# Optimization experiments

Measured on AMD Instinct MI355X. Metric: run time of the kernel, lower is better.

## Reference

```python
import math
import jax, jax.numpy as jnp
import numpy as np

B, T, D = 8, 2048, 1024

def _gelu(x):
    # tanh-approx GELU, matching the torch module's _gelu
    c = math.sqrt(2.0 / math.pi)
    return 0.5 * x * (1.0 + jnp.tanh(c * (x + 0.044715 * x * x * x)))

def _normalize(x, axis):
    # matches F.normalize(eps=1e-12)
    n = jnp.linalg.norm(x, axis=axis, keepdims=True)
    return x / jnp.maximum(n, 1e-12)

def setup_inputs() -> dict:
    key = jax.random.key(0)
    k1, k2 = jax.random.split(key)
    x = jax.random.normal(k1, (B, T, D), dtype=jnp.float32)
    ema_out = _normalize(jax.random.normal(k2, (D,), dtype=jnp.float32), 0)[..., 0] if False else None
    ema = jax.random.normal(k2, (D,), dtype=jnp.float32)
    ema = ema / jnp.maximum(jnp.linalg.norm(ema), 1e-12)
    return {
        "x": x,
        "ema_out": ema,
        "logit_decay": jnp.float32(math.log(0.9 / 0.1)),
        "log_tau": jnp.float32(math.log(2.0)),
        "log_blend": jnp.float32(math.log(0.3 / 0.7)),
        "logit_blend_seq": jnp.float32(0.0),
    }

def reference(x, ema_out, logit_decay, log_tau, log_blend, logit_blend_seq):
    Bx, Tx, Dx = x.shape
    tau = jnp.exp(log_tau)
    alpha = jax.nn.sigmoid(log_blend)
    w_seq = jax.nn.sigmoid(logit_blend_seq)

    out = _gelu(x)                              # [B,T,D]
    out_norm = _normalize(out, -1)              # [B,T,D]
    ema_norm = ema_out / jnp.maximum(jnp.linalg.norm(ema_out), 1e-12)  # [D]

    ema_sim = jnp.einsum('btd,d->bt', out_norm, ema_norm)             # [B,T]
    sim_mat = jnp.einsum('btd,bsd->bts', out_norm, out_norm)          # [B,T,T]

    causal = jnp.tril(jnp.ones((Tx, Tx), dtype=bool), k=-1)           # strict past
    sim_past = jnp.where(causal[None], sim_mat, -2.0)
    seq_sim = jnp.max(sim_past, axis=-1)                              # [B,T]

    has_past = (jnp.arange(Tx) > 0)[None, :]                          # [1,T]
    seq_sim = jnp.where(has_past, seq_sim, ema_sim)

    familiarity = w_seq * seq_sim + (1.0 - w_seq) * ema_sim
    novelty = jnp.exp(-tau * familiarity)
    gate = 1.0 - alpha + alpha * novelty                              # [B,T]
    return out * gate[..., None]
```

## Files before the change

kernel.cpp:

```cpp
#include <hip/hip_runtime.h>
#include <math.h>

#define NB 8
#define TT 2048
#define DD 1024
#define NTI 16
#define NPAIR 136

typedef __attribute__((ext_vector_type(4))) float floatx4;

__device__ inline float fast_gelu(float x) {
    float z = 0.7978845608028654f * (x + 0.044715f * x * x * x);
    float e = __expf(2.0f * z);
    float th = 1.0f - 2.0f / (e + 1.0f);
    return 0.5f * x * (1.0f + th);
}

__global__ __launch_bounds__(256) void k_gelu_norm(
        const float* __restrict__ x, const float* __restrict__ ema,
        unsigned int* __restrict__ onrm8, float* __restrict__ ema_sim) {
    int row = blockIdx.x * 4 + (threadIdx.x >> 6);
    int lane = threadIdx.x & 63;
    const float4* xr = reinterpret_cast<const float4*>(x + (size_t)row * DD);
    const float4* er = reinterpret_cast<const float4*>(ema);
    float g[16];
    float ss = 0.f, dt = 0.f, e2 = 0.f;
#pragma unroll
    for (int j = 0; j < 4; ++j) {
        float4 v = xr[j * 64 + lane];
        float4 e = er[j * 64 + lane];
        float vv[4] = {v.x, v.y, v.z, v.w};
        float ee[4] = {e.x, e.y, e.z, e.w};
        e2 += ee[0] * ee[0] + ee[1] * ee[1] + ee[2] * ee[2] + ee[3] * ee[3];
#pragma unroll
        for (int i = 0; i < 4; ++i) {
            float o = fast_gelu(vv[i]);
            g[j * 4 + i] = o;
            ss += o * o;
            dt += o * ee[i];
        }
    }
#pragma unroll
    for (int m = 1; m < 64; m <<= 1) {
        ss += __shfl_xor(ss, m);
        dt += __shfl_xor(dt, m);
        e2 += __shfl_xor(e2, m);
    }
    float inv = 1.0f / fmaxf(sqrtf(ss), 1e-12f);
    float einv = 1.0f / fmaxf(sqrtf(e2), 1e-12f);
    unsigned int* o8 = onrm8 + (size_t)row * (DD / 4);
#pragma unroll
    for (int j = 0; j < 4; ++j) {
        int pk = 0;
        pk = __builtin_amdgcn_cvt_pk_fp8_f32(g[j * 4 + 0] * inv, g[j * 4 + 1] * inv, pk, false);
        pk = __builtin_amdgcn_cvt_pk_fp8_f32(g[j * 4 + 2] * inv, g[j * 4 + 3] * inv, pk, true);
        o8[j * 64 + lane] = (unsigned int)pk;
    }
    if (lane == 0) ema_sim[row] = dt * inv * einv;
}

__global__ __launch_bounds__(256) void k_seqmax(const unsigned char* __restrict__ onrm8,
                                                float* __restrict__ part) {
    __shared__ __align__(16) unsigned char lds[32768];

    int id = blockIdx.x;
    int nid = (id & 7) * NPAIR + (id >> 3);
    int b = nid / NPAIR;
    int p = nid % NPAIR;
    int ti = (int)((sqrtf(8.0f * (float)p + 1.0f) - 1.0f) * 0.5f);
    while ((ti + 1) * (ti + 2) / 2 <= p) ++ti;
    while (ti * (ti + 1) / 2 > p) --ti;
    int sj = p - ti * (ti + 1) / 2;

    int lane = threadIdx.x & 63;
    int wave = threadIdx.x >> 6;
    int wr = wave >> 1, wc = wave & 1;
    int rl = lane & 15, g = lane >> 4;

    const unsigned char* Abase = onrm8 + (size_t)(b * TT + ti * 128) * DD;
    const unsigned char* Bbase = onrm8 + (size_t)(b * TT + sj * 128) * DD;

    floatx4 acc[4][4];
#pragma unroll
    for (int i = 0; i < 4; i++)
#pragma unroll
        for (int j = 0; j < 4; j++) acc[i][j] = (floatx4){0.f, 0.f, 0.f, 0.f};

    auto stage = [&](int kt) {
#pragma unroll
        for (int i = 0; i < 4; ++i) {
            int c = wave * 4 + i;
            int off = c * 1024 + lane * 16;
            int row = off >> 7;
            int colb = (off & 127) ^ ((row & 7) << 4);
            const unsigned char* srcA = Abase + (size_t)row * DD + kt * 128 + colb;
            const unsigned char* srcB = Bbase + (size_t)row * DD + kt * 128 + colb;
            __builtin_amdgcn_global_load_lds(
                (const __attribute__((address_space(1))) unsigned int*)srcA,
                (__attribute__((address_space(3))) unsigned int*)(&lds[0] + c * 1024),
                16, 0, 0);
            __builtin_amdgcn_global_load_lds(
                (const __attribute__((address_space(1))) unsigned int*)srcB,
                (__attribute__((address_space(3))) unsigned int*)(&lds[16384] + c * 1024),
                16, 0, 0);
        }
    };

    auto ldfrag = [&](const unsigned char* base, int r, int ks) -> long {
        int sw = (r & 7) << 4;
        return *(const long*)(base + r * 128 + ((ks * 32 + g * 8) ^ sw));
    };

    for (int kt = 0; kt < 8; ++kt) {
        stage(kt);
        __syncthreads();
#pragma unroll
        for (int ks = 0; ks < 4; ++ks) {
            long af[4], bg[4];
#pragma unroll
            for (int f = 0; f < 4; ++f) {
                af[f] = ldfrag(&lds[0], wr * 64 + f * 16 + rl, ks);
                bg[f] = ldfrag(&lds[16384], wc * 64 + f * 16 + rl, ks);
            }
#pragma unroll
            for (int fi = 0; fi < 4; ++fi)
#pragma unroll
                for (int fj = 0; fj < 4; ++fj)
                    acc[fi][fj] = __builtin_amdgcn_mfma_f32_16x16x32_fp8_fp8(
                        af[fi], bg[fj], acc[fi][fj], 0, 0, 0);
        }
        __syncthreads();
    }

    int t0g = ti * 128 + wr * 64;
    int s0g = sj * 128 + wc * 64;
#pragma unroll
    for (int fi = 0; fi < 4; ++fi) {
#pragma unroll
        for (int r = 0; r < 4; ++r) {
            int trow = t0g + fi * 16 + g * 4 + r;
            float m = -2.0f;
#pragma unroll
            for (int fj = 0; fj < 4; ++fj) {
                int scol = s0g + fj * 16 + rl;
                m = fmaxf(m, (scol < trow) ? acc[fi][fj][r] : -2.0f);
            }
#pragma unroll
            for (int msk = 1; msk < 16; msk <<= 1) m = fmaxf(m, __shfl_xor(m, msk));
            if (rl == 0)
                part[(((size_t)b * 32 + sj * 2 + wc) << 11) + trow] = m;
        }
    }
}

__global__ __launch_bounds__(256) void k_gate(
        const float* __restrict__ x, float* __restrict__ out,
        const float* __restrict__ ema_sim, const float* __restrict__ part,
        const float* __restrict__ log_tau,
        const float* __restrict__ log_blend,
        const float* __restrict__ logit_blend_seq) {
    int row = blockIdx.x * 4 + (threadIdx.x >> 6);
    int lane = threadIdx.x & 63;
    int b = row >> 11;
    int t = row & (TT - 1);

    int n = 2 * ((t >> 7) + 1);
    float m = (lane < n) ? part[(((size_t)b * 32 + lane) << 11) + t] : -2.0f;
#pragma unroll
    for (int msk = 1; msk < 64; msk <<= 1) m = fmaxf(m, __shfl_xor(m, msk));

    float tau = __expf(log_tau[0]);
    float alpha = 1.f / (1.f + __expf(-log_blend[0]));
    float wseq = 1.f / (1.f + __expf(-logit_blend_seq[0]));
    float es = ema_sim[row];
    float sq = (t > 0) ? m : es;
    float fam = wseq * sq + (1.f - wseq) * es;
    float gate = 1.f - alpha + alpha * __expf(-tau * fam);

    const float4* xr = reinterpret_cast<const float4*>(x + (size_t)row * DD);
    float4* orow = reinterpret_cast<float4*>(out + (size_t)row * DD);
#pragma unroll
    for (int j = 0; j < 4; ++j) {
        float4 v = xr[j * 64 + lane];
        float4 o;
        o.x = fast_gelu(v.x) * gate;
        o.y = fast_gelu(v.y) * gate;
        o.z = fast_gelu(v.z) * gate;
        o.w = fast_gelu(v.w) * gate;
        orow[j * 64 + lane] = o;
    }
}

extern "C" void kernel_launch(void* const* d_in, const int* in_sizes, int n_in,
                              void* d_out, int out_size, void* d_ws, size_t ws_size,
                              hipStream_t stream) {
    const float* x = (const float*)d_in[0];
    const float* ema = (const float*)d_in[1];
    const float* log_tau = (const float*)d_in[3];
    const float* log_blend = (const float*)d_in[4];
    const float* logit_bs = (const float*)d_in[5];
    float* out = (float*)d_out;

    char* ws = (char*)d_ws;
    float* ema_sim = (float*)(ws + (4 << 10));
    float* part = (float*)(ws + (132 << 10));
    unsigned char* onrm8 = (unsigned char*)(ws + ((size_t)2304 << 10));

    k_gelu_norm<<<NB * TT / 4, 256, 0, stream>>>(x, ema, (unsigned int*)onrm8, ema_sim);
    k_seqmax<<<NB * NPAIR, 256, 0, stream>>>(onrm8, part);
    k_gate<<<NB * TT / 4, 256, 0, stream>>>(x, out, ema_sim, part,
                                            log_tau, log_blend, logit_bs);
}
```

Before: 90.12 us.

## Use single-wave 64x64 tiles with double-buffered LDS prefetch in seqmax

The causal similarity-max kernel now launches one wave per block, each computing a 64x64 lower-triangular tile, instead of four waves sharing a 128x128 tile. Without cross-wave sharing the block barriers go away, and the next K slice is prefetched into a second LDS buffer with explicit vmcnt waits so loads overlap MFMA work. The smaller tiles waste less compute on the diagonal and give more blocks, but each block reuses its loaded data less, so global/L2 traffic rises. The gate kernel is updated to reduce over 64-row partials.

```diff
diff --git a/kernel.cpp b/kernel.cpp
--- a/kernel.cpp
+++ b/kernel.cpp
@@ -4,8 +4,8 @@
 #define NB 8
 #define TT 2048
 #define DD 1024
-#define NTI 16
-#define NPAIR 136
+#define NT64 32
+#define NP64 528
 
 typedef __attribute__((ext_vector_type(4))) float floatx4;
 
@@ -59,26 +59,24 @@
     if (lane == 0) ema_sim[row] = dt * inv * einv;
 }
 
-__global__ __launch_bounds__(256) void k_seqmax(const unsigned char* __restrict__ onrm8,
-                                                float* __restrict__ part) {
-    __shared__ __align__(16) unsigned char lds[32768];
+__global__ __launch_bounds__(64) void k_seqmax(const unsigned char* __restrict__ onrm8,
+                                               float* __restrict__ part) {
+    __shared__ __align__(16) unsigned char lds[2][16384];
 
     int id = blockIdx.x;
-    int nid = (id & 7) * NPAIR + (id >> 3);
-    int b = nid / NPAIR;
-    int p = nid % NPAIR;
+    int nid = (id & 7) * NP64 + (id >> 3);
+    int b = nid / NP64;
+    int p = nid % NP64;
     int ti = (int)((sqrtf(8.0f * (float)p + 1.0f) - 1.0f) * 0.5f);
     while ((ti + 1) * (ti + 2) / 2 <= p) ++ti;
     while (ti * (ti + 1) / 2 > p) --ti;
     int sj = p - ti * (ti + 1) / 2;
 
-    int lane = threadIdx.x & 63;
-    int wave = threadIdx.x >> 6;
-    int wr = wave >> 1, wc = wave & 1;
+    int lane = threadIdx.x;
     int rl = lane & 15, g = lane >> 4;
 
-    const unsigned char* Abase = onrm8 + (size_t)(b * TT + ti * 128) * DD;
-    const unsigned char* Bbase = onrm8 + (size_t)(b * TT + sj * 128) * DD;
+    const unsigned char* Abase = onrm8 + (size_t)(b * TT + ti * 64) * DD;
+    const unsigned char* Bbase = onrm8 + (size_t)(b * TT + sj * 64) * DD;
 
     floatx4 acc[4][4];
 #pragma unroll
@@ -86,41 +84,47 @@
 #pragma unroll
         for (int j = 0; j < 4; j++) acc[i][j] = (floatx4){0.f, 0.f, 0.f, 0.f};
 
-    auto stage = [&](int kt) {
-#pragma unroll
-        for (int i = 0; i < 4; ++i) {
-            int c = wave * 4 + i;
-            int off = c * 1024 + lane * 16;
+    auto stage = [&](int buf, int kt) {
+#pragma unroll
+        for (int i = 0; i < 8; ++i) {
+            int off = i * 1024 + lane * 16;
             int row = off >> 7;
             int colb = (off & 127) ^ ((row & 7) << 4);
             const unsigned char* srcA = Abase + (size_t)row * DD + kt * 128 + colb;
             const unsigned char* srcB = Bbase + (size_t)row * DD + kt * 128 + colb;
             __builtin_amdgcn_global_load_lds(
                 (const __attribute__((address_space(1))) unsigned int*)srcA,
-                (__attribute__((address_space(3))) unsigned int*)(&lds[0] + c * 1024),
+                (__attribute__((address_space(3))) unsigned int*)(&lds[buf][0] + i * 1024),
                 16, 0, 0);
             __builtin_amdgcn_global_load_lds(
                 (const __attribute__((address_space(1))) unsigned int*)srcB,
-                (__attribute__((address_space(3))) unsigned int*)(&lds[16384] + c * 1024),
+                (__attribute__((address_space(3))) unsigned int*)(&lds[buf][8192] + i * 1024),
                 16, 0, 0);
         }
     };
 
-    auto ldfrag = [&](const unsigned char* base, int r, int ks) -> long {
-        int sw = (r & 7) << 4;
-        return *(const long*)(base + r * 128 + ((ks * 32 + g * 8) ^ sw));
-    };
-
+    stage(0, 0);
     for (int kt = 0; kt < 8; ++kt) {
-        stage(kt);
-        __syncthreads();
+        int buf = kt & 1;
+        if (kt + 1 < 8) {
+            stage(buf ^ 1, kt + 1);
+            asm volatile("s_waitcnt vmcnt(16)" ::: "memory");
+        } else {
+            asm volatile("s_waitcnt vmcnt(0)" ::: "memory");
+        }
+        __builtin_amdgcn_sched_barrier(0);
+        const unsigned char* Ab = &lds[buf][0];
+        const unsigned char* Bb = &lds[buf][8192];
 #pragma unroll
         for (int ks = 0; ks < 4; ++ks) {
             long af[4], bg[4];
+            int cb = ks * 32 + g * 8;
+            int sw = (rl & 7) << 4;
 #pragma unroll
             for (int f = 0; f < 4; ++f) {
-                af[f] = ldfrag(&lds[0], wr * 64 + f * 16 + rl, ks);
-                bg[f] = ldfrag(&lds[16384], wc * 64 + f * 16 + rl, ks);
+                int r = f * 16 + rl;
+                af[f] = *(const long*)(Ab + r * 128 + (cb ^ sw));
+                bg[f] = *(const long*)(Bb + r * 128 + (cb ^ sw));
             }
 #pragma unroll
             for (int fi = 0; fi < 4; ++fi)
@@ -129,11 +133,10 @@
                     acc[fi][fj] = __builtin_amdgcn_mfma_f32_16x16x32_fp8_fp8(
                         af[fi], bg[fj], acc[fi][fj], 0, 0, 0);
         }
-        __syncthreads();
-    }
-
-    int t0g = ti * 128 + wr * 64;
-    int s0g = sj * 128 + wc * 64;
+    }
+
+    int t0g = ti * 64;
+    int s0g = sj * 64;
 #pragma unroll
     for (int fi = 0; fi < 4; ++fi) {
 #pragma unroll
@@ -148,7 +151,7 @@
 #pragma unroll
             for (int msk = 1; msk < 16; msk <<= 1) m = fmaxf(m, __shfl_xor(m, msk));
             if (rl == 0)
-                part[(((size_t)b * 32 + sj * 2 + wc) << 11) + trow] = m;
+                part[(((size_t)b * 32 + sj) << 11) + trow] = m;
         }
     }
 }
@@ -164,7 +167,7 @@
     int b = row >> 11;
     int t = row & (TT - 1);
 
-    int n = 2 * ((t >> 7) + 1);
+    int n = (t >> 6) + 1;
     float m = (lane < n) ? part[(((size_t)b * 32 + lane) << 11) + t] : -2.0f;
 #pragma unroll
     for (int msk = 1; msk < 64; msk <<= 1) m = fmaxf(m, __shfl_xor(m, msk));
@@ -207,7 +210,7 @@
     unsigned char* onrm8 = (unsigned char*)(ws + ((size_t)2304 << 10));
 
     k_gelu_norm<<<NB * TT / 4, 256, 0, stream>>>(x, ema, (unsigned int*)onrm8, ema_sim);
-    k_seqmax<<<NB * NPAIR, 256, 0, stream>>>(onrm8, part);
+    k_seqmax<<<NB * NP64, 64, 0, stream>>>(onrm8, part);
     k_gate<<<NB * TT / 4, 256, 0, stream>>>(x, out, ema_sim, part,
                                             log_tau, log_blend, logit_bs);
 }
```

After: 96.96 us. 1.08x slower.
